# Kernel optimization log

Hardware: AMD Instinct MI355X
Metric: run time of the kernel (lower is better)

The kernel has to match this reference:

```python
import jax, jax.numpy as jnp
import numpy as np

N_NODES, N_FEAT, HIDDEN, N_CLASSES, N_EDGES = 100000, 64, 64, 16, 1600000


def setup_inputs() -> dict:
    key = jax.random.key(0)
    ks = jax.random.split(key, 10)
    x = jax.random.normal(ks[0], (N_NODES, N_FEAT), dtype=jnp.float32)
    edge_index = jax.random.randint(ks[1], (2, N_EDGES), 0, N_NODES, dtype=jnp.int32)
    edge_weight = jax.random.uniform(ks[2], (N_EDGES,), dtype=jnp.float32)
    # Glorot-style init for GCNConv weights, zero bias (as in torch_geometric)
    W1 = jax.random.normal(ks[3], (N_FEAT, HIDDEN), dtype=jnp.float32) / np.float32(np.sqrt(N_FEAT))
    b1 = jnp.zeros((HIDDEN,), jnp.float32)
    W2 = jax.random.normal(ks[4], (HIDDEN, HIDDEN), dtype=jnp.float32) / np.float32(np.sqrt(HIDDEN))
    b2 = jnp.zeros((HIDDEN,), jnp.float32)
    W3 = jax.random.normal(ks[5], (HIDDEN, N_CLASSES), dtype=jnp.float32) / np.float32(np.sqrt(HIDDEN))
    b3 = jnp.zeros((N_CLASSES,), jnp.float32)
    return {"x": x, "edge_index": edge_index, "edge_weight": edge_weight,
            "W1": W1, "b1": b1, "W2": W2, "b2": b2, "W3": W3, "b3": b3}


def _gcn_norm(edge_index, edge_weight, num_nodes):
    """Add self-loops (weight 1) and compute symmetric D^-1/2 A D^-1/2 norm."""
    loop = jnp.arange(num_nodes, dtype=edge_index.dtype)
    src = jnp.concatenate([edge_index[0], loop])
    dst = jnp.concatenate([edge_index[1], loop])
    ew = jnp.concatenate([edge_weight, jnp.ones((num_nodes,), edge_weight.dtype)])
    deg = jax.ops.segment_sum(ew, dst, num_segments=num_nodes)
    dis = jnp.where(deg > 0, jax.lax.rsqrt(jnp.where(deg > 0, deg, 1.0)), 0.0)
    norm = dis[src] * ew * dis[dst]  # [E+N]
    return src, dst, norm


def reference(x, edge_index, edge_weight, W1, b1, W2, b2, W3, b3):
    N = x.shape[0]
    src, dst, norm = _gcn_norm(edge_index, edge_weight, N)

    def conv(h, W, b):
        hw = h @ W                                   # [N, out]
        msg = norm[:, None] * hw[src]                # [E+N, out]
        return jax.ops.segment_sum(msg, dst, num_segments=N) + b

    # conv1 + ReLU (dropout is identity in eval mode)
    h = jax.nn.relu(conv(x, W1, b1))
    # one hidden GCNConv layer (num_layer=3)
    h = jax.nn.relu(conv(h, W2, b2))
    logits = conv(h, W3, b3)                         # [N, C]
    out = jax.nn.log_softmax(logits, axis=1)
    return (out, logits, logits)
```

## Files before the change

### kernel.cpp

```cpp
#include <hip/hip_runtime.h>
#include <hip/hip_bf16.h>

#define N_FEAT 64
#define NBW 9
#define SRC_BITS 23

typedef unsigned short u16;
typedef __attribute__((ext_vector_type(8))) short short8;
typedef __attribute__((ext_vector_type(4))) float f32x4;

__device__ inline u16 f2bf(float f) {
    unsigned u = __float_as_uint(f);
    u += 0x7fffu + ((u >> 16) & 1u);
    return (u16)(u >> 16);
}


__global__ __launch_bounds__(256) void coarse_hist(const int* __restrict__ ei, int* bcnt, int E, int NB) {
    __shared__ int h[256];
    int tid = threadIdx.x;
    h[tid] = 0;
    __syncthreads();
    for (int e = blockIdx.x * blockDim.x + tid; e < E; e += gridDim.x * blockDim.x)
        atomicAdd(&h[ei[E + e] >> NBW], 1);
    __syncthreads();
    if (tid < NB && h[tid]) atomicAdd(&bcnt[tid], h[tid]);
}

__device__ inline void packW(const float* __restrict__ W, uint4* __restrict__ Wpk,
                             int ncb, int wcols, int tid) {
    int nf = ncb * 2 * 64;
    for (int f = tid; f < nf; f += 256) {
        int cb = f >> 7;
        int s  = (f >> 6) & 1;
        int lane = f & 63;
        int kb = lane >> 4, c16 = lane & 15;
        union { uint4 q; u16 u[8]; } pk;
        #pragma unroll
        for (int i = 0; i < 8; ++i) {
            int k = s * 32 + kb * 8 + i;
            pk.u[i] = f2bf(W[k * wcols + cb * 16 + c16]);
        }
        Wpk[f] = pk.q;
    }
}

__global__ __launch_bounds__(256) void scan_pad(const int* __restrict__ bcnt, int* boff, int* bcur, int NB,
                                                const float* __restrict__ W1, const float* __restrict__ W2,
                                                const float* __restrict__ W3,
                                                uint4* Wp1, uint4* Wp2, uint4* Wp3) {
    if (blockIdx.x == 0) {
        __shared__ int wsum[4];
        int tid = threadIdx.x, lane = tid & 63, w = tid >> 6;
        int v = (tid < NB) ? bcnt[tid] : 0;
        int incl = v;
        #pragma unroll
        for (int o = 1; o < 64; o <<= 1) { int t = __shfl_up(incl, o); if (lane >= o) incl += t; }
        if (lane == 63) wsum[w] = incl;
        __syncthreads();
        int add = 0;
        #pragma unroll
        for (int i = 0; i < 4; ++i) if (i < w) add += wsum[i];
        int excl = add + incl - v;
        if (tid < NB) { boff[tid] = excl; bcur[tid] = excl; }
    } else if (blockIdx.x == 1) {
        packW(W1, Wp1, 4, 64, threadIdx.x);
    } else if (blockIdx.x == 2) {
        packW(W2, Wp2, 4, 64, threadIdx.x);
    } else {
        packW(W3, Wp3, 1, 16, threadIdx.x);
    }
}

__global__ __launch_bounds__(256) void partition(const int* __restrict__ ei, const float* __restrict__ ew,
                                                 int* bcur, int2* __restrict__ ebuf, int E, int NB) {
    constexpr int EPT = 8;
    __shared__ int cnt[256];
    __shared__ int base[256];
    int tid = threadIdx.x;
    cnt[tid] = 0;
    __syncthreads();
    int start = blockIdx.x * (256 * EPT);

    int d[EPT], r[EPT], s[EPT]; float w[EPT];
    #pragma unroll
    for (int i = 0; i < EPT; ++i) {
        int e = start + i * 256 + tid;
        if (e < E) {
            d[i] = ei[E + e];
            s[i] = ei[e];
            w[i] = ew[e];
            r[i] = atomicAdd(&cnt[d[i] >> NBW], 1);
        } else d[i] = -1;
    }
    __syncthreads();
    if (tid < NB && cnt[tid]) base[tid] = atomicAdd(&bcur[tid], cnt[tid]);
    __syncthreads();
    #pragma unroll
    for (int i = 0; i < EPT; ++i) {
        if (d[i] >= 0) {
            int b = d[i] >> NBW;
            int dl = d[i] & ((1 << NBW) - 1);
            int key = (dl << SRC_BITS) | s[i];
            ebuf[base[b] + r[i]] = make_int2(key, __float_as_int(w[i]));
        }
    }
}

__global__ __launch_bounds__(256) void bucket_csr(const int2* __restrict__ ebuf, const int* __restrict__ boff,
                                                  const int* __restrict__ bcnt,
                                                  int2* __restrict__ csr, int* __restrict__ rowp,
                                                  int* __restrict__ cnt, float* __restrict__ dis, int N) {
    __shared__ int   h[512];
    __shared__ float ws[512];
    __shared__ int   off[512];
    __shared__ int   wsum[4];
    int b = blockIdx.x, tid = threadIdx.x;
    int nbase = b << NBW;
    int nn = min(512, N - nbase);
    int beg = boff[b], m = bcnt[b];

    h[tid] = 0; h[tid + 256] = 0;
    ws[tid] = 0.f; ws[tid + 256] = 0.f;
    __syncthreads();

    for (int i = tid; i < m; i += 256) {
        int2 en = ebuf[beg + i];
        int dl = ((unsigned)en.x) >> SRC_BITS;
        atomicAdd(&h[dl], 1);
        atomicAdd(&ws[dl], __int_as_float(en.y));
    }
    __syncthreads();

    int v0 = h[2 * tid], v1 = h[2 * tid + 1];
    int v = v0 + v1;
    int lane = tid & 63, wv = tid >> 6;
    int incl = v;
    #pragma unroll
    for (int o = 1; o < 64; o <<= 1) { int t = __shfl_up(incl, o); if (lane >= o) incl += t; }
    if (lane == 63) wsum[wv] = incl;
    __syncthreads();
    int add = 0;
    #pragma unroll
    for (int i = 0; i < 4; ++i) if (i < wv) add += wsum[i];
    int excl = add + incl - v;
    off[2 * tid] = excl;
    off[2 * tid + 1] = excl + v0;
    __syncthreads();

    for (int l = tid; l < nn; l += 256) {
        rowp[nbase + l] = beg + off[l];
        cnt[nbase + l]  = h[l];
        dis[nbase + l]  = rsqrtf(1.0f + ws[l]);
    }
    __syncthreads();
    h[tid] = 0; h[tid + 256] = 0;
    __syncthreads();

    for (int i = tid; i < m; i += 256) {
        int2 en = ebuf[beg + i];
        unsigned k = (unsigned)en.x;
        int dl  = k >> SRC_BITS;
        int src = k & ((1 << SRC_BITS) - 1);
        int pos = atomicAdd(&h[dl], 1);
        csr[beg + off[dl] + pos] = make_int2(src, en.y);
    }
}


template<int OUTW, bool INBF>
__global__ __launch_bounds__(256) void gemm_mf(const void* __restrict__ Av, const uint4* __restrict__ Wpk,
                                               const float* __restrict__ dis,
                                               u16* __restrict__ C, int N) {
    constexpr int NCB = OUTW / 16;
    int lane = threadIdx.x & 63;
    int wid  = (int)((blockIdx.x * blockDim.x + threadIdx.x) >> 6);
    int r0 = wid * 16;
    if (r0 >= N) return;
    int row16 = lane & 15, kb = lane >> 4;
    int r = min(r0 + row16, N - 1);

    short8 a0, a1;
    if (INBF) {
        const u16* arow = (const u16*)Av + (size_t)r * 64 + kb * 8;
        a0 = __builtin_bit_cast(short8, *(const uint4*)arow);
        a1 = __builtin_bit_cast(short8, *(const uint4*)(arow + 32));
    } else {
        const float* arow = (const float*)Av + (size_t)r * 64 + kb * 8;
        float4 f0 = *(const float4*)arow;
        float4 f1 = *(const float4*)(arow + 4);
        float4 f2 = *(const float4*)(arow + 32);
        float4 f3 = *(const float4*)(arow + 36);
        union { short8 v; u16 u[8]; } pa, pb;
        pa.u[0] = f2bf(f0.x); pa.u[1] = f2bf(f0.y); pa.u[2] = f2bf(f0.z); pa.u[3] = f2bf(f0.w);
        pa.u[4] = f2bf(f1.x); pa.u[5] = f2bf(f1.y); pa.u[6] = f2bf(f1.z); pa.u[7] = f2bf(f1.w);
        pb.u[0] = f2bf(f2.x); pb.u[1] = f2bf(f2.y); pb.u[2] = f2bf(f2.z); pb.u[3] = f2bf(f2.w);
        pb.u[4] = f2bf(f3.x); pb.u[5] = f2bf(f3.y); pb.u[6] = f2bf(f3.z); pb.u[7] = f2bf(f3.w);
        a0 = pa.v; a1 = pb.v;
    }

    f32x4 acc[NCB];
    #pragma unroll
    for (int cb = 0; cb < NCB; ++cb) {
        short8 b0 = __builtin_bit_cast(short8, Wpk[(cb * 2 + 0) * 64 + lane]);
        short8 b1 = __builtin_bit_cast(short8, Wpk[(cb * 2 + 1) * 64 + lane]);
        f32x4 z = {0.f, 0.f, 0.f, 0.f};
        z = __builtin_amdgcn_mfma_f32_16x16x32_bf16(a0, b0, z, 0, 0, 0);
        z = __builtin_amdgcn_mfma_f32_16x16x32_bf16(a1, b1, z, 0, 0, 0);
        acc[cb] = z;
    }

    int rbase = r0 + kb * 4;
    float dsc[4];
    #pragma unroll
    for (int j = 0; j < 4; ++j) dsc[j] = dis[min(rbase + j, N - 1)];

    #pragma unroll
    for (int cb = 0; cb < NCB; ++cb) {
        int col = cb * 16 + row16;
        #pragma unroll
        for (int j = 0; j < 4; ++j) {
            int rr = rbase + j;
            if (rr < N) C[(size_t)rr * OUTW + col] = f2bf(acc[cb][j] * dsc[j]);
        }
    }
}


template<int F, bool RELU, bool FINAL>
__global__ __launch_bounds__(256) void aggregate(const u16* __restrict__ hw, const int* __restrict__ rowp,
                                                 const int* __restrict__ cnt, const int2* __restrict__ csr,
                                                 const float* __restrict__ dis,
                                                 const float* __restrict__ bias, void* __restrict__ outv,
                                                 float* __restrict__ out2, float* __restrict__ out3, int N) {
    constexpr int GL   = F / 8;
    constexpr int NPW  = 64 / GL;
    constexpr unsigned ROWB = F * 2;
    constexpr int UN   = 8;

    int wv   = (int)((blockIdx.x * blockDim.x + threadIdx.x) >> 6);
    int lane = threadIdx.x & 63;
    int g = lane / GL;
    int t = lane % GL;
    int n = wv * NPW + g;
    bool alive = (n < N);
    n = min(n, N - 1);

    float dd = dis[n];
    int beg = rowp[n];
    int c   = cnt[n];
    const char* hwb = (const char*)hw;
    unsigned toff = (unsigned)t * 16u;

    float acc[8];
    {
        uint4 raw = *(const uint4*)(hwb + (unsigned)n * ROWB + toff);
        unsigned uw[4] = {raw.x, raw.y, raw.z, raw.w};
        #pragma unroll
        for (int k = 0; k < 4; ++k) {
            acc[2 * k]     = __uint_as_float(uw[k] << 16);
            acc[2 * k + 1] = __uint_as_float(uw[k] & 0xffff0000u);
        }
    }

    for (int j0 = 0; j0 < c; j0 += UN) {
        int2 e[UN];
        #pragma unroll
        for (int i = 0; i < UN; ++i) e[i] = csr[beg + min(j0 + i, c - 1)];
        uint4 r[UN]; float w[UN];
        #pragma unroll
        for (int i = 0; i < UN; ++i) {
            r[i] = *(const uint4*)(hwb + (unsigned)e[i].x * ROWB + toff);
            w[i] = (j0 + i < c) ? __int_as_float(e[i].y) : 0.0f;
        }
        #pragma unroll
        for (int i = 0; i < UN; ++i) {
            unsigned u[4] = {r[i].x, r[i].y, r[i].z, r[i].w};
            #pragma unroll
            for (int k = 0; k < 4; ++k) {
                acc[2 * k]     = fmaf(w[i], __uint_as_float(u[k] << 16), acc[2 * k]);
                acc[2 * k + 1] = fmaf(w[i], __uint_as_float(u[k] & 0xffff0000u), acc[2 * k + 1]);
            }
        }
    }

    if (alive) {
        float4 b0 = *(const float4*)&bias[t * 8];
        float4 b1 = *(const float4*)&bias[t * 8 + 4];
        float bb[8] = {b0.x, b0.y, b0.z, b0.w, b1.x, b1.y, b1.z, b1.w};
        #pragma unroll
        for (int k = 0; k < 8; ++k) acc[k] = fmaf(dd, acc[k], bb[k]);
        if (RELU) {
            #pragma unroll
            for (int k = 0; k < 8; ++k) acc[k] = fmaxf(acc[k], 0.0f);
        }
        if (!FINAL) {
            u16* o16 = (u16*)outv;
            uint4 pk;
            pk.x = (unsigned)f2bf(acc[0]) | ((unsigned)f2bf(acc[1]) << 16);
            pk.y = (unsigned)f2bf(acc[2]) | ((unsigned)f2bf(acc[3]) << 16);
            pk.z = (unsigned)f2bf(acc[4]) | ((unsigned)f2bf(acc[5]) << 16);
            pk.w = (unsigned)f2bf(acc[6]) | ((unsigned)f2bf(acc[7]) << 16);
            *(uint4*)&o16[(size_t)n * F + t * 8] = pk;
        } else {
            float4 r0 = make_float4(acc[0], acc[1], acc[2], acc[3]);
            float4 r1 = make_float4(acc[4], acc[5], acc[6], acc[7]);
            *(float4*)&out2[(size_t)n * F + t * 8] = r0;
            *(float4*)&out2[(size_t)n * F + t * 8 + 4] = r1;
            *(float4*)&out3[(size_t)n * F + t * 8] = r0;
            *(float4*)&out3[(size_t)n * F + t * 8 + 4] = r1;
            float mloc = acc[0];
            #pragma unroll
            for (int k = 1; k < 8; ++k) mloc = fmaxf(mloc, acc[k]);
            float m = fmaxf(mloc, __shfl_xor(mloc, 1));
            float sloc = 0.f;
            #pragma unroll
            for (int k = 0; k < 8; ++k) sloc += __expf(acc[k] - m);
            float ssum = sloc + __shfl_xor(sloc, 1);
            float ls = m + __logf(ssum);
            float* o = (float*)outv;
            float4 w0 = make_float4(acc[0] - ls, acc[1] - ls, acc[2] - ls, acc[3] - ls);
            float4 w1 = make_float4(acc[4] - ls, acc[5] - ls, acc[6] - ls, acc[7] - ls);
            *(float4*)&o[(size_t)n * F + t * 8] = w0;
            *(float4*)&o[(size_t)n * F + t * 8 + 4] = w1;
        }
    }
}


extern "C" void kernel_launch(void* const* d_in, const int* in_sizes, int n_in,
                              void* d_out, int out_size, void* d_ws, size_t ws_size,
                              hipStream_t stream) {
    const float* x   = (const float*)d_in[0];
    const int*   ei  = (const int*)d_in[1];
    const float* ew  = (const float*)d_in[2];
    const float* W1  = (const float*)d_in[3];
    const float* b1  = (const float*)d_in[4];
    const float* W2  = (const float*)d_in[5];
    const float* b2  = (const float*)d_in[6];
    const float* W3  = (const float*)d_in[7];
    const float* b3  = (const float*)d_in[8];
    float* out = (float*)d_out;

    const int N = in_sizes[0] / N_FEAT;
    const int E = in_sizes[2];
    const int NB = (N + (1 << NBW) - 1) >> NBW;

    size_t off = 0;
    auto alloc = [&](size_t bytes) {
        void* p = (char*)d_ws + off;
        off += (bytes + 255) & ~(size_t)255;
        return p;
    };
    float* dis     = (float*)alloc((size_t)N * 4);
    int*   cnt     = (int*)alloc((size_t)N * 4);
    int*   rowp    = (int*)alloc((size_t)N * 4);
    int*   bcnt    = (int*)alloc(256 * 4);
    int*   boff    = (int*)alloc(256 * 4);
    int*   bcur    = (int*)alloc(256 * 4);
    int2*  csr     = (int2*)alloc((size_t)E * 8);
    int2*  ebuf    = (int2*)alloc((size_t)E * 8);
    u16*   bufA16  = (u16*)alloc((size_t)N * 64 * 2);
    u16*   hwB     = (u16*)alloc((size_t)N * 64 * 2);
    u16*   hw16    = (u16*)alloc((size_t)N * 16 * 2);
    uint4* Wp1     = (uint4*)alloc(512 * 16);
    uint4* Wp2     = (uint4*)alloc(512 * 16);
    uint4* Wp3     = (uint4*)alloc(128 * 16);

    const int TB = 256;

    hipMemsetAsync(bcnt, 0, 256 * 4, stream);
    coarse_hist<<<512, TB, 0, stream>>>(ei, bcnt, E, NB);
    scan_pad<<<4, TB, 0, stream>>>(bcnt, boff, bcur, NB, W1, W2, W3, Wp1, Wp2, Wp3);
    partition<<<(E + 2047) / 2048, TB, 0, stream>>>(ei, ew, bcur, ebuf, E, NB);
    bucket_csr<<<NB, TB, 0, stream>>>(ebuf, boff, bcnt, csr, rowp, cnt, dis, N);

    int gblk   = ((N + 15) / 16 + 3) / 4;
    int ablk64 = (N * 8 + TB - 1) / TB;
    int ablk16 = (N * 2 + TB - 1) / TB;

    float* logits = out + (size_t)N * 16;
    float* logits2 = out + (size_t)2 * N * 16;

    gemm_mf<64, false><<<gblk, TB, 0, stream>>>(x, Wp1, dis, hwB, N);
    aggregate<64, true, false><<<ablk64, TB, 0, stream>>>(hwB, rowp, cnt, csr, dis, b1, bufA16, nullptr, nullptr, N);
    gemm_mf<64, true><<<gblk, TB, 0, stream>>>(bufA16, Wp2, dis, hwB, N);
    aggregate<64, true, false><<<ablk64, TB, 0, stream>>>(hwB, rowp, cnt, csr, dis, b2, bufA16, nullptr, nullptr, N);
    gemm_mf<16, true><<<gblk, TB, 0, stream>>>(bufA16, Wp3, dis, hw16, N);
    aggregate<16, false, true><<<ablk16, TB, 0, stream>>>(hw16, rowp, cnt, csr, dis, b3, out, logits, logits2, N);
}
```

Baseline: 193.2 us.

## Overlap first GEMM with edge partition and split aggregation rows across half-waves

The first-layer GEMM no longer depends on the degree normalisation. It now runs unscaled inside the same launch as the edge partition kernel, so it overlaps with the sort and one launch goes away. The first aggregation compensates by multiplying each edge weight by dis[src] with an extra gather, and by scaling the self term. All aggregations now give each node's edge list to two half-waves that process alternating chunks and combine their sums with a cross-lane shuffle, which doubles the thread count for more memory parallelism. The cost is an extra dis gather per edge in layer one and more launched threads.

```diff
diff --git a/kernel.cpp b/kernel.cpp
--- a/kernel.cpp
+++ b/kernel.cpp
@@ -72,109 +72,12 @@
     }
 }
 
-__global__ __launch_bounds__(256) void partition(const int* __restrict__ ei, const float* __restrict__ ew,
-                                                 int* bcur, int2* __restrict__ ebuf, int E, int NB) {
-    constexpr int EPT = 8;
-    __shared__ int cnt[256];
-    __shared__ int base[256];
-    int tid = threadIdx.x;
-    cnt[tid] = 0;
-    __syncthreads();
-    int start = blockIdx.x * (256 * EPT);
-
-    int d[EPT], r[EPT], s[EPT]; float w[EPT];
-    #pragma unroll
-    for (int i = 0; i < EPT; ++i) {
-        int e = start + i * 256 + tid;
-        if (e < E) {
-            d[i] = ei[E + e];
-            s[i] = ei[e];
-            w[i] = ew[e];
-            r[i] = atomicAdd(&cnt[d[i] >> NBW], 1);
-        } else d[i] = -1;
-    }
-    __syncthreads();
-    if (tid < NB && cnt[tid]) base[tid] = atomicAdd(&bcur[tid], cnt[tid]);
-    __syncthreads();
-    #pragma unroll
-    for (int i = 0; i < EPT; ++i) {
-        if (d[i] >= 0) {
-            int b = d[i] >> NBW;
-            int dl = d[i] & ((1 << NBW) - 1);
-            int key = (dl << SRC_BITS) | s[i];
-            ebuf[base[b] + r[i]] = make_int2(key, __float_as_int(w[i]));
-        }
-    }
-}
-
-__global__ __launch_bounds__(256) void bucket_csr(const int2* __restrict__ ebuf, const int* __restrict__ boff,
-                                                  const int* __restrict__ bcnt,
-                                                  int2* __restrict__ csr, int* __restrict__ rowp,
-                                                  int* __restrict__ cnt, float* __restrict__ dis, int N) {
-    __shared__ int   h[512];
-    __shared__ float ws[512];
-    __shared__ int   off[512];
-    __shared__ int   wsum[4];
-    int b = blockIdx.x, tid = threadIdx.x;
-    int nbase = b << NBW;
-    int nn = min(512, N - nbase);
-    int beg = boff[b], m = bcnt[b];
-
-    h[tid] = 0; h[tid + 256] = 0;
-    ws[tid] = 0.f; ws[tid + 256] = 0.f;
-    __syncthreads();
-
-    for (int i = tid; i < m; i += 256) {
-        int2 en = ebuf[beg + i];
-        int dl = ((unsigned)en.x) >> SRC_BITS;
-        atomicAdd(&h[dl], 1);
-        atomicAdd(&ws[dl], __int_as_float(en.y));
-    }
-    __syncthreads();
-
-    int v0 = h[2 * tid], v1 = h[2 * tid + 1];
-    int v = v0 + v1;
-    int lane = tid & 63, wv = tid >> 6;
-    int incl = v;
-    #pragma unroll
-    for (int o = 1; o < 64; o <<= 1) { int t = __shfl_up(incl, o); if (lane >= o) incl += t; }
-    if (lane == 63) wsum[wv] = incl;
-    __syncthreads();
-    int add = 0;
-    #pragma unroll
-    for (int i = 0; i < 4; ++i) if (i < wv) add += wsum[i];
-    int excl = add + incl - v;
-    off[2 * tid] = excl;
-    off[2 * tid + 1] = excl + v0;
-    __syncthreads();
-
-    for (int l = tid; l < nn; l += 256) {
-        rowp[nbase + l] = beg + off[l];
-        cnt[nbase + l]  = h[l];
-        dis[nbase + l]  = rsqrtf(1.0f + ws[l]);
-    }
-    __syncthreads();
-    h[tid] = 0; h[tid + 256] = 0;
-    __syncthreads();
-
-    for (int i = tid; i < m; i += 256) {
-        int2 en = ebuf[beg + i];
-        unsigned k = (unsigned)en.x;
-        int dl  = k >> SRC_BITS;
-        int src = k & ((1 << SRC_BITS) - 1);
-        int pos = atomicAdd(&h[dl], 1);
-        csr[beg + off[dl] + pos] = make_int2(src, en.y);
-    }
-}
-
-
-template<int OUTW, bool INBF>
-__global__ __launch_bounds__(256) void gemm_mf(const void* __restrict__ Av, const uint4* __restrict__ Wpk,
-                                               const float* __restrict__ dis,
-                                               u16* __restrict__ C, int N) {
+
+template<int OUTW, bool INBF, bool SCALE>
+__device__ inline void gemm_body(const void* __restrict__ Av, const uint4* __restrict__ Wpk,
+                                 const float* __restrict__ dis, u16* __restrict__ C, int N,
+                                 int wid, int lane) {
     constexpr int NCB = OUTW / 16;
-    int lane = threadIdx.x & 63;
-    int wid  = (int)((blockIdx.x * blockDim.x + threadIdx.x) >> 6);
     int r0 = wid * 16;
     if (r0 >= N) return;
     int row16 = lane & 15, kb = lane >> 4;
@@ -213,7 +116,7 @@
     int rbase = r0 + kb * 4;
     float dsc[4];
     #pragma unroll
-    for (int j = 0; j < 4; ++j) dsc[j] = dis[min(rbase + j, N - 1)];
+    for (int j = 0; j < 4; ++j) dsc[j] = SCALE ? dis[min(rbase + j, N - 1)] : 1.0f;
 
     #pragma unroll
     for (int cb = 0; cb < NCB; ++cb) {
@@ -221,28 +124,144 @@
         #pragma unroll
         for (int j = 0; j < 4; ++j) {
             int rr = rbase + j;
-            if (rr < N) C[(size_t)rr * OUTW + col] = f2bf(acc[cb][j] * dsc[j]);
-        }
-    }
-}
-
-
-template<int F, bool RELU, bool FINAL>
+            if (rr < N) C[(size_t)rr * OUTW + col] = f2bf(SCALE ? acc[cb][j] * dsc[j] : acc[cb][j]);
+        }
+    }
+}
+
+template<int OUTW, bool INBF, bool SCALE>
+__global__ __launch_bounds__(256) void gemm_mf(const void* __restrict__ Av, const uint4* __restrict__ Wpk,
+                                               const float* __restrict__ dis,
+                                               u16* __restrict__ C, int N) {
+    int lane = threadIdx.x & 63;
+    int wid  = (int)((blockIdx.x * blockDim.x + threadIdx.x) >> 6);
+    gemm_body<OUTW, INBF, SCALE>(Av, Wpk, dis, C, N, wid, lane);
+}
+
+
+__global__ __launch_bounds__(256) void part_gemm(const int* __restrict__ ei, const float* __restrict__ ew,
+                                                 int* bcur, int2* __restrict__ ebuf, int E, int NB, int PB,
+                                                 const float* __restrict__ x, const uint4* __restrict__ Wp1,
+                                                 u16* __restrict__ hwB, int N) {
+    constexpr int EPT = 8;
+    __shared__ int cnt[256];
+    __shared__ int base[256];
+    int tid = threadIdx.x;
+
+    if ((int)blockIdx.x >= PB) {
+        int wid = (int)(((blockIdx.x - PB) * blockDim.x + tid) >> 6);
+        gemm_body<64, false, false>(x, Wp1, nullptr, hwB, N, wid, tid & 63);
+        return;
+    }
+
+    cnt[tid] = 0;
+    __syncthreads();
+    int start = blockIdx.x * (256 * EPT);
+
+    int d[EPT], r[EPT], s[EPT]; float w[EPT];
+    #pragma unroll
+    for (int i = 0; i < EPT; ++i) {
+        int e = start + i * 256 + tid;
+        if (e < E) {
+            d[i] = ei[E + e];
+            s[i] = ei[e];
+            w[i] = ew[e];
+            r[i] = atomicAdd(&cnt[d[i] >> NBW], 1);
+        } else d[i] = -1;
+    }
+    __syncthreads();
+    if (tid < NB && cnt[tid]) base[tid] = atomicAdd(&bcur[tid], cnt[tid]);
+    __syncthreads();
+    #pragma unroll
+    for (int i = 0; i < EPT; ++i) {
+        if (d[i] >= 0) {
+            int b = d[i] >> NBW;
+            int dl = d[i] & ((1 << NBW) - 1);
+            int key = (dl << SRC_BITS) | s[i];
+            ebuf[base[b] + r[i]] = make_int2(key, __float_as_int(w[i]));
+        }
+    }
+}
+
+__global__ __launch_bounds__(256) void bucket_csr(const int2* __restrict__ ebuf, const int* __restrict__ boff,
+                                                  const int* __restrict__ bcnt,
+                                                  int2* __restrict__ csr, int* __restrict__ rowp,
+                                                  int* __restrict__ cnt, float* __restrict__ dis, int N) {
+    __shared__ int   h[512];
+    __shared__ float ws[512];
+    __shared__ int   off[512];
+    __shared__ int   wsum[4];
+    int b = blockIdx.x, tid = threadIdx.x;
+    int nbase = b << NBW;
+    int nn = min(512, N - nbase);
+    int beg = boff[b], m = bcnt[b];
+
+    h[tid] = 0; h[tid + 256] = 0;
+    ws[tid] = 0.f; ws[tid + 256] = 0.f;
+    __syncthreads();
+
+    for (int i = tid; i < m; i += 256) {
+        int2 en = ebuf[beg + i];
+        int dl = ((unsigned)en.x) >> SRC_BITS;
+        atomicAdd(&h[dl], 1);
+        atomicAdd(&ws[dl], __int_as_float(en.y));
+    }
+    __syncthreads();
+
+    int v0 = h[2 * tid], v1 = h[2 * tid + 1];
+    int v = v0 + v1;
+    int lane = tid & 63, wv = tid >> 6;
+    int incl = v;
+    #pragma unroll
+    for (int o = 1; o < 64; o <<= 1) { int t = __shfl_up(incl, o); if (lane >= o) incl += t; }
+    if (lane == 63) wsum[wv] = incl;
+    __syncthreads();
+    int add = 0;
+    #pragma unroll
+    for (int i = 0; i < 4; ++i) if (i < wv) add += wsum[i];
+    int excl = add + incl - v;
+    off[2 * tid] = excl;
+    off[2 * tid + 1] = excl + v0;
+    __syncthreads();
+
+    for (int l = tid; l < nn; l += 256) {
+        rowp[nbase + l] = beg + off[l];
+        cnt[nbase + l]  = h[l];
+        dis[nbase + l]  = rsqrtf(1.0f + ws[l]);
+    }
+    __syncthreads();
+    h[tid] = 0; h[tid + 256] = 0;
+    __syncthreads();
+
+    for (int i = tid; i < m; i += 256) {
+        int2 en = ebuf[beg + i];
+        unsigned k = (unsigned)en.x;
+        int dl  = k >> SRC_BITS;
+        int src = k & ((1 << SRC_BITS) - 1);
+        int pos = atomicAdd(&h[dl], 1);
+        csr[beg + off[dl] + pos] = make_int2(src, en.y);
+    }
+}
+
+
+template<int F, bool RELU, bool FINAL, bool LOADDIS>
 __global__ __launch_bounds__(256) void aggregate(const u16* __restrict__ hw, const int* __restrict__ rowp,
                                                  const int* __restrict__ cnt, const int2* __restrict__ csr,
                                                  const float* __restrict__ dis,
                                                  const float* __restrict__ bias, void* __restrict__ outv,
                                                  float* __restrict__ out2, float* __restrict__ out3, int N) {
     constexpr int GL   = F / 8;
-    constexpr int NPW  = 64 / GL;
+    constexpr int NPW  = 32 / GL;
     constexpr unsigned ROWB = F * 2;
     constexpr int UN   = 8;
 
     int wv   = (int)((blockIdx.x * blockDim.x + threadIdx.x) >> 6);
     int lane = threadIdx.x & 63;
-    int g = lane / GL;
-    int t = lane % GL;
-    int n = wv * NPW + g;
+    int s = lane >> 5;
+    int wl = lane & 31;
+    int q = wl / GL;
+    int t = wl % GL;
+    int n = wv * NPW + q;
     bool alive = (n < N);
     n = min(n, N - 1);
 
@@ -255,15 +274,16 @@
     float acc[8];
     {
         uint4 raw = *(const uint4*)(hwb + (unsigned)n * ROWB + toff);
+        float sw = (s == 0) ? (LOADDIS ? dd : 1.0f) : 0.0f;
         unsigned uw[4] = {raw.x, raw.y, raw.z, raw.w};
         #pragma unroll
         for (int k = 0; k < 4; ++k) {
-            acc[2 * k]     = __uint_as_float(uw[k] << 16);
-            acc[2 * k + 1] = __uint_as_float(uw[k] & 0xffff0000u);
-        }
-    }
-
-    for (int j0 = 0; j0 < c; j0 += UN) {
+            acc[2 * k]     = sw * __uint_as_float(uw[k] << 16);
+            acc[2 * k + 1] = sw * __uint_as_float(uw[k] & 0xffff0000u);
+        }
+    }
+
+    for (int j0 = s * UN; j0 < c; j0 += 2 * UN) {
         int2 e[UN];
         #pragma unroll
         for (int i = 0; i < UN; ++i) e[i] = csr[beg + min(j0 + i, c - 1)];
@@ -271,7 +291,9 @@
         #pragma unroll
         for (int i = 0; i < UN; ++i) {
             r[i] = *(const uint4*)(hwb + (unsigned)e[i].x * ROWB + toff);
-            w[i] = (j0 + i < c) ? __int_as_float(e[i].y) : 0.0f;
+            float wr = __int_as_float(e[i].y);
+            if (LOADDIS) wr *= dis[e[i].x];
+            w[i] = (j0 + i < c) ? wr : 0.0f;
         }
         #pragma unroll
         for (int i = 0; i < UN; ++i) {
@@ -284,7 +306,10 @@
         }
     }
 
-    if (alive) {
+    #pragma unroll
+    for (int k = 0; k < 8; ++k) acc[k] += __shfl_xor(acc[k], 32);
+
+    if (alive && s == 0) {
         float4 b0 = *(const float4*)&bias[t * 8];
         float4 b1 = *(const float4*)&bias[t * 8 + 4];
         float bb[8] = {b0.x, b0.y, b0.z, b0.w, b1.x, b1.y, b1.z, b1.w};
@@ -369,23 +394,24 @@
 
     const int TB = 256;
 
+    int gblk = ((N + 15) / 16 + 3) / 4;
+    int PB   = (E + 2047) / 2048;
+
     hipMemsetAsync(bcnt, 0, 256 * 4, stream);
     coarse_hist<<<512, TB, 0, stream>>>(ei, bcnt, E, NB);
     scan_pad<<<4, TB, 0, stream>>>(bcnt, boff, bcur, NB, W1, W2, W3, Wp1, Wp2, Wp3);
-    partition<<<(E + 2047) / 2048, TB, 0, stream>>>(ei, ew, bcur, ebuf, E, NB);
+    part_gemm<<<PB + gblk, TB, 0, stream>>>(ei, ew, bcur, ebuf, E, NB, PB, x, Wp1, hwB, N);
     bucket_csr<<<NB, TB, 0, stream>>>(ebuf, boff, bcnt, csr, rowp, cnt, dis, N);
 
-    int gblk   = ((N + 15) / 16 + 3) / 4;
-    int ablk64 = (N * 8 + TB - 1) / TB;
-    int ablk16 = (N * 2 + TB - 1) / TB;
+    int ablk64 = (N * 16 + TB - 1) / TB;
+    int ablk16 = (N * 4 + TB - 1) / TB;
 
     float* logits = out + (size_t)N * 16;
     float* logits2 = out + (size_t)2 * N * 16;
 
-    gemm_mf<64, false><<<gblk, TB, 0, stream>>>(x, Wp1, dis, hwB, N);
-    aggregate<64, true, false><<<ablk64, TB, 0, stream>>>(hwB, rowp, cnt, csr, dis, b1, bufA16, nullptr, nullptr, N);
-    gemm_mf<64, true><<<gblk, TB, 0, stream>>>(bufA16, Wp2, dis, hwB, N);
-    aggregate<64, true, false><<<ablk64, TB, 0, stream>>>(hwB, rowp, cnt, csr, dis, b2, bufA16, nullptr, nullptr, N);
-    gemm_mf<16, true><<<gblk, TB, 0, stream>>>(bufA16, Wp3, dis, hw16, N);
-    aggregate<16, false, true><<<ablk16, TB, 0, stream>>>(hw16, rowp, cnt, csr, dis, b3, out, logits, logits2, N);
-}
+    aggregate<64, true, false, true><<<ablk64, TB, 0, stream>>>(hwB, rowp, cnt, csr, dis, b1, bufA16, nullptr, nullptr, N);
+    gemm_mf<64, true, true><<<gblk, TB, 0, stream>>>(bufA16, Wp2, dis, hwB, N);
+    aggregate<64, true, false, false><<<ablk64, TB, 0, stream>>>(hwB, rowp, cnt, csr, dis, b2, bufA16, nullptr, nullptr, N);
+    gemm_mf<16, true, true><<<gblk, TB, 0, stream>>>(bufA16, Wp3, dis, hw16, N);
+    aggregate<16, false, true, false><<<ablk16, TB, 0, stream>>>(hw16, rowp, cnt, csr, dis, b3, out, logits, logits2, N);
+}
```

Measured after the change: 192.1 us. About the same (-0.5%).
